# Kernel tuning notes

Hardware: AMD Instinct MI355X
Metric: run time of the kernel (lower is better)

## Reference

```python
import math
import jax, jax.numpy as jnp
import numpy as np

H = 4  # num heads
D = 512
MLP = 1024
EPS = 1e-6


def _ln(x, g, b):
    m = x.mean(-1, keepdims=True)
    v = ((x - m) ** 2).mean(-1, keepdims=True)
    return (x - m) / jnp.sqrt(v + EPS) * g + b


def _heads(x):
    B, S, d = x.shape
    return x.reshape(B, S, H, d // H).transpose(0, 2, 1, 3)  # [B,H,S,hd]


def _att(q, k, v, Wo, bo):
    # q,k,v: [B,S,D] already projected
    hd = q.shape[-1] // H
    qh, kh, vh = _heads(q), _heads(k), _heads(v)
    scores = jnp.einsum('bhqd,bhkd->bhqk', qh, kh) / math.sqrt(hd)
    probs = jax.nn.softmax(scores, axis=-1)
    ctx = jnp.einsum('bhqk,bhkd->bhqd', probs, vh)
    B, _, S, _ = ctx.shape
    ctx = ctx.transpose(0, 2, 1, 3).reshape(B, S, H * hd)
    return ctx @ Wo + bo


def setup_inputs() -> dict:
    key = jax.random.key(0)
    ks = jax.random.split(key, 32)
    i = iter(range(32))
    def w(shape, scale=0.02):
        return jax.random.normal(ks[next(i)], shape, dtype=jnp.float32) * scale
    inp = {
        'x1': jax.random.normal(ks[next(i)], (16, 1024, D), dtype=jnp.float32),
        'x2': jax.random.normal(ks[next(i)], (16, 1024, D), dtype=jnp.float32),
        'ln1_g': jnp.ones((D,), jnp.float32), 'ln1_b': jnp.zeros((D,), jnp.float32),
        'ln2_g': jnp.ones((D,), jnp.float32), 'ln2_b': jnp.zeros((D,), jnp.float32),
        'lnf_g': jnp.ones((D,), jnp.float32), 'lnf_b': jnp.zeros((D,), jnp.float32),
    }
    for name in ['q1', 'k1', 'v1', 'q2', 'k2', 'v2', 'q12', 'k12', 'v12', 'o']:
        inp['W' + name] = w((D, D))
        inp['b' + name] = jnp.zeros((D,), jnp.float32)
    inp['W1'] = w((D, MLP)); inp['b1'] = jnp.zeros((MLP,), jnp.float32)
    inp['W2'] = w((MLP, D)); inp['b2'] = jnp.zeros((D,), jnp.float32)
    return inp


def reference(x1, x2, ln1_g, ln1_b, ln2_g, ln2_b, lnf_g, lnf_b,
              Wq1, bq1, Wk1, bk1, Wv1, bv1,
              Wq2, bq2, Wk2, bk2, Wv2, bv2,
              Wq12, bq12, Wk12, bk12, Wv12, bv12,
              Wo, bo, W1, b1, W2, b2):
    identity = x1
    x1n = _ln(x1, ln1_g, ln1_b)
    x2n = _ln(x2, ln2_g, ln2_b)
    # stream-1 self-attention with residual onto normalized input
    src1 = x1n + _att(x1n @ Wq1 + bq1, x1n @ Wk1 + bk1, x1n @ Wv1 + bv1, Wo, bo)
    # stream-2 self-attention
    src2 = x2n + _att(x2n @ Wq2 + bq2, x2n @ Wk2 + bk2, x2n @ Wv2 + bv2, Wo, bo)
    # cross attention: query from src1, key/value from src2
    attn_out = _att(src1 @ Wq12 + bq12, src2 @ Wk12 + bk12, src2 @ Wv12 + bv12, Wo, bo)
    x = attn_out + identity
    h = _ln(x, lnf_g, lnf_b)
    h = jax.nn.gelu(h @ W1 + b1, approximate=False) @ W2 + b2
    return x + h
```

## Files before the change

### kernel.cpp

```cpp
#include <hip/hip_runtime.h>
#include <math.h>


#define SEQ   1024
#define DM    512
#define HDIM  128
#define MTOK  16384
#define MLPD  1024
#define SC2   ((float)(0.08838834764831845 * 1.4426950408889634))

typedef short bf16x8 __attribute__((ext_vector_type(8)));
typedef float f32x4  __attribute__((ext_vector_type(4)));
typedef float f32x16 __attribute__((ext_vector_type(16)));
typedef unsigned short us4 __attribute__((ext_vector_type(4)));

typedef unsigned int u32g __attribute__((address_space(1)));
typedef unsigned int u32l __attribute__((address_space(3)));

static __device__ __forceinline__ unsigned short f2b(float f) {
  union { float f; unsigned u; } v; v.f = f;
  unsigned r = v.u + 0x7FFFu + ((v.u >> 16) & 1u);
  return (unsigned short)(r >> 16);
}
static __device__ __forceinline__ float b2f(unsigned short h) {
  union { unsigned u; float f; } v; v.u = ((unsigned)h) << 16;
  return v.f;
}
static __device__ __forceinline__ unsigned pk2t(float a, float b) {
  union { float f; unsigned u; } va, vb; va.f = a; vb.f = b;
  return __builtin_amdgcn_perm(vb.u, va.u, 0x07060302u);
}
static __device__ __forceinline__ void gl_lds16(const void* g, void* l) {
  __builtin_amdgcn_global_load_lds((u32g*)g, (u32l*)l, 16, 0, 0);
}

struct P12 { const float* p[12]; };
struct P9  { const float* p[9]; };

__global__ __launch_bounds__(256) void prep_kernel(P12 ws, P9 bs,
                                                   unsigned short* __restrict__ WT0,
                                                   unsigned short* __restrict__ W1t,
                                                   unsigned short* __restrict__ W2t,
                                                   float* __restrict__ bcc) {
  int bid = blockIdx.x;
  if (bid >= 3584) {
    int i = (bid - 3584) * 256 + threadIdx.x;
    if (i < 4608) bcc[i] = bs.p[i >> 9][i & 511];
    return;
  }
  __shared__ float t[32][33];
  const float* W; unsigned short* Wt; int K, N, tt;
  if (bid < 2560)      { int wi = bid >> 8; W = ws.p[wi]; Wt = WT0 + (size_t)wi * 262144; K = 512; N = 512; tt = bid & 255; }
  else if (bid < 3072) { W = ws.p[10]; Wt = W1t; K = 512;  N = 1024; tt = bid - 2560; }
  else                 { W = ws.p[11]; Wt = W2t; K = 1024; N = 512;  tt = bid - 3072; }
  int ntiles = N >> 5;
  int bx = tt % ntiles, by = tt / ntiles;
  int n0 = bx * 32, k0 = by * 32;
  int tx = threadIdx.x & 31, ty = threadIdx.x >> 5;
#pragma unroll
  for (int i = 0; i < 32; i += 8)
    t[ty + i][tx] = W[(size_t)(k0 + ty + i) * N + n0 + tx];
  __syncthreads();
#pragma unroll
  for (int i = 0; i < 32; i += 8)
    Wt[(size_t)(n0 + ty + i) * K + k0 + tx] = f2b(t[tx][ty + i]);
}

__global__ __launch_bounds__(256) void ln_kernel(const float* __restrict__ X0,
                                                 const float* __restrict__ X1,
                                                 const float* __restrict__ g0w,
                                                 const float* __restrict__ b0w,
                                                 const float* __restrict__ g1w,
                                                 const float* __restrict__ b1w,
                                                 unsigned short* __restrict__ out0,
                                                 unsigned short* __restrict__ out1) {
  int idx  = blockIdx.x * 4 + (threadIdx.x >> 6);
  int sel  = idx >> 14;
  int row  = idx & 16383;
  const float* X = sel ? X1 : X0;
  const float* gw = sel ? g1w : g0w;
  const float* bw = sel ? b1w : b0w;
  unsigned short* outB = sel ? out1 : out0;
  int lane = threadIdx.x & 63;
  const float4* xr = (const float4*)(X + (size_t)row * DM);
  float4 a = xr[lane];
  float4 c = xr[lane + 64];
  float s  = a.x + a.y + a.z + a.w + c.x + c.y + c.z + c.w;
  float s2 = a.x*a.x + a.y*a.y + a.z*a.z + a.w*a.w
           + c.x*c.x + c.y*c.y + c.z*c.z + c.w*c.w;
#pragma unroll
  for (int off = 1; off < 64; off <<= 1) {
    s  += __shfl_xor(s,  off, 64);
    s2 += __shfl_xor(s2, off, 64);
  }
  float mean = s * (1.0f / 512.0f);
  float var  = s2 * (1.0f / 512.0f) - mean * mean;
  float rstd = rsqrtf(var + 1e-6f);
  const float4* gv = (const float4*)gw;
  const float4* bv = (const float4*)bw;
  float4 g1 = gv[lane], g2 = gv[lane + 64];
  float4 b1 = bv[lane], b2 = bv[lane + 64];
  us4 o1, o2;
  o1.x = f2b((a.x - mean) * rstd * g1.x + b1.x);
  o1.y = f2b((a.y - mean) * rstd * g1.y + b1.y);
  o1.z = f2b((a.z - mean) * rstd * g1.z + b1.z);
  o1.w = f2b((a.w - mean) * rstd * g1.w + b1.w);
  o2.x = f2b((c.x - mean) * rstd * g2.x + b2.x);
  o2.y = f2b((c.y - mean) * rstd * g2.y + b2.y);
  o2.z = f2b((c.z - mean) * rstd * g2.z + b2.z);
  o2.w = f2b((c.w - mean) * rstd * g2.w + b2.w);
  *(us4*)(outB + (size_t)row * DM + lane * 4)        = o1;
  *(us4*)(outB + (size_t)row * DM + (lane + 64) * 4) = o2;
}

template <int RES, bool GELU_ACT, int OMODE>
__global__ __launch_bounds__(256, 2) void gemm_kernel(const unsigned short* __restrict__ A,
                                                      const unsigned short* __restrict__ A1,
                                                      const unsigned short* __restrict__ Bt,
                                                      const float* __restrict__ bias,
                                                      const void* __restrict__ res,
                                                      float* __restrict__ outF,
                                                      unsigned short* __restrict__ outB,
                                                      unsigned short* __restrict__ outV,
                                                      int M, int N, int K) {
  int nT = N >> 7;
  int mT = M >> 7;
  int xcd = blockIdx.x & 7;
  int idx = blockIdx.x >> 3;
  int mPerX = mT >> 3;
  int q = idx / nT;
  int tm = xcd * mPerX + q;
  int tn = idx - q * nT;
  int m0 = tm << 7, n0 = tn << 7;
  int tid = threadIdx.x, lane = tid & 63, w = tid >> 6;
  int m16 = lane & 15, q4 = lane >> 4;
  int wr = (w & 1) << 6, wc = (w >> 1) << 6;
  __shared__ unsigned short Alds[2][128 * 64];
  __shared__ unsigned short Blds[2][128 * 64];
  f32x4 acc[4][4] = {};

  const unsigned short* Aeff = A;
  const unsigned short* Bteff = Bt;
  const float* biaseff = bias;
  if (OMODE == 3) {
    int half = tm >> 7;
    Bteff = Bt + (size_t)half * 3 * 262144;
    biaseff = bias + half * 1536;
  }
  if (OMODE == 4) {
    if (tn >= 4) Aeff = A1;
  }

  int srow = lane >> 3;
  int scol = ((lane & 7) ^ srow) << 3;
  const unsigned short* Ag = Aeff  + (size_t)(m0 + w * 8 + srow) * K + scol;
  const unsigned short* Bg = Bteff + (size_t)(n0 + w * 8 + srow) * K + scol;
  int ldst = w * 512;

#pragma unroll
  for (int it = 0; it < 4; ++it) {
    gl_lds16(Ag + (size_t)it * 32 * K, Alds[0] + it * 2048 + ldst);
    gl_lds16(Bg + (size_t)it * 32 * K, Blds[0] + it * 2048 + ldst);
  }

  int nk = K >> 6;
  for (int ks = 0; ks < nk; ++ks) {
    int cur = ks & 1, nxt = cur ^ 1;
    __syncthreads();
    if (ks + 1 < nk) {
      int k0n = (ks + 1) << 6;
#pragma unroll
      for (int it = 0; it < 4; ++it) {
        gl_lds16(Ag + (size_t)it * 32 * K + k0n, Alds[nxt] + it * 2048 + ldst);
        gl_lds16(Bg + (size_t)it * 32 * K + k0n, Blds[nxt] + it * 2048 + ldst);
      }
    }
    const unsigned short* Ar = Alds[cur];
    const unsigned short* Br = Blds[cur];
#pragma unroll
    for (int kk = 0; kk < 64; kk += 32) {
      bf16x8 af[4], bfr[4];
#pragma unroll
      for (int i = 0; i < 4; ++i) {
        int row = wr + i * 16 + m16;
        af[i] = *(const bf16x8*)(Ar + row * 64 + ((((kk >> 3) + q4) ^ (m16 & 7)) << 3));
      }
#pragma unroll
      for (int j = 0; j < 4; ++j) {
        int row = wc + j * 16 + m16;
        bfr[j] = *(const bf16x8*)(Br + row * 64 + ((((kk >> 3) + q4) ^ (m16 & 7)) << 3));
      }
#pragma unroll
      for (int i = 0; i < 4; ++i)
#pragma unroll
        for (int j = 0; j < 4; ++j)
          acc[i][j] = __builtin_amdgcn_mfma_f32_16x16x32_bf16(af[i], bfr[j], acc[i][j], 0, 0, 0);
    }
  }
  if (OMODE == 3 || OMODE == 4) {
    if (n0 < 1024) {
      int stride = (OMODE == 3) ? 1024 : 512;
      unsigned short* ob = outB;
      int coff = 0;
      if (OMODE == 4 && n0 >= 512) { ob = outB + (size_t)MTOK * 512; coff = 512; }
      float sc = (n0 < 512) ? SC2 : 1.0f;
#pragma unroll
      for (int i = 0; i < 4; ++i) {
#pragma unroll
        for (int r = 0; r < 4; ++r) {
          int row = m0 + wr + i * 16 + q4 * 4 + r;
#pragma unroll
          for (int j = 0; j < 4; ++j) {
            int col = n0 + wc + j * 16 + m16;
            ob[(size_t)row * stride + col - coff] = f2b((acc[i][j][r] + biaseff[col]) * sc);
          }
        }
      }
    } else {
#pragma unroll
      for (int i = 0; i < 4; ++i) {
        int row0 = m0 + wr + i * 16 + q4 * 4;
        int s = row0 & 1023, bl = row0 >> 10;
        s = (s & ~12) | ((s & 4) << 1) | ((s & 8) >> 1);
#pragma unroll
        for (int j = 0; j < 4; ++j) {
          int col = n0 + wc + j * 16 + m16;
          int hh = (col - 1024) >> 7, hd = col & 127;
          float bb = biaseff[col];
          us4 pkv;
          pkv.x = f2b(acc[i][j][0] + bb);
          pkv.y = f2b(acc[i][j][1] + bb);
          pkv.z = f2b(acc[i][j][2] + bb);
          pkv.w = f2b(acc[i][j][3] + bb);
          *(us4*)(outV + (((size_t)(bl * 4 + hh)) * HDIM + hd) * SEQ + s) = pkv;
        }
      }
    }
  } else {
#pragma unroll
    for (int i = 0; i < 4; ++i) {
#pragma unroll
      for (int r = 0; r < 4; ++r) {
        int row = m0 + wr + i * 16 + q4 * 4 + r;
#pragma unroll
        for (int j = 0; j < 4; ++j) {
          int col = n0 + wc + j * 16 + m16;
          float v = acc[i][j][r] + bias[col];
          if (RES == 1) v += ((const float*)res)[(size_t)row * N + col];
          if (RES == 2) v += b2f(((const unsigned short*)res)[(size_t)row * N + col]);
          if (GELU_ACT) v = 0.5f * v * (1.0f + erff(v * 0.70710678118654752f));
          if (OMODE == 1) outF[(size_t)row * N + col] = v;
          else            outB[(size_t)row * N + col] = f2b(v);
        }
      }
    }
  }
}

__global__ __launch_bounds__(256, 2) void attn_kernel(const unsigned short* __restrict__ Qb_,
                                                      const unsigned short* __restrict__ Kb_,
                                                      int tstride,
                                                      const unsigned short* __restrict__ Vt,
                                                      unsigned short* __restrict__ CTX,
                                                      int pairs_per_xcd) {
  int xcd = blockIdx.x & 7;
  int i   = blockIdx.x >> 3;
  int pair = xcd * pairs_per_xcd + (i >> 3);
  int qt   = i & 7;
  int b = pair >> 2, h = pair & 3;
  int tid = threadIdx.x, lane = tid & 63, w = tid >> 6;
  int m32 = lane & 31, hf = lane >> 5;
  size_t qkoff = ((size_t)b * SEQ) * tstride + h * HDIM;
  const unsigned short* Qg = Qb_ + qkoff;
  const unsigned short* Kg = Kb_ + qkoff;
  const unsigned short* Vp = Vt + (size_t)pair * HDIM * SEQ;

  __shared__ unsigned short Klds[2][64 * 128];
  __shared__ unsigned short Vlds[2][128 * 64];

  int qrow0 = qt * 128 + w * 32;
  bf16x8 qf[8];
  {
    const unsigned short* qp = Qg + (size_t)(qrow0 + m32) * tstride + hf * 8;
#pragma unroll
    for (int ks = 0; ks < 8; ++ks) qf[ks] = *(const bf16x8*)(qp + ks * 16);
  }
  bf16x8 onesf;
#pragma unroll
  for (int j = 0; j < 8; ++j) onesf[j] = (short)0x3F80;

  const unsigned short* kp0 = Kg + (size_t)(16 * w + (lane >> 4)) * tstride
                              + (((lane & 15) ^ (lane >> 4)) << 3);
  const unsigned short* kp1 = Kg + (size_t)(16 * w + 4 + (lane >> 4)) * tstride
                              + (((lane & 15) ^ ((lane >> 4) + 4)) << 3);
  const unsigned short* vp0 = Vp + (size_t)(32 * w + (lane >> 3)) * SEQ
                              + (((lane & 7) ^ (lane >> 3)) << 3);
  int klo = 16 * w * 128;
  int vlo = 32 * w * 64;

  gl_lds16(kp0,               Klds[0] + klo);
  gl_lds16(kp1,               Klds[0] + klo + 4 * 128);
  gl_lds16(kp0 + 8 * tstride, Klds[0] + klo + 8 * 128);
  gl_lds16(kp1 + 8 * tstride, Klds[0] + klo + 12 * 128);
  gl_lds16(vp0,               Vlds[0] + vlo);
  gl_lds16(vp0 + 8 * SEQ,     Vlds[0] + vlo + 8 * 64);
  gl_lds16(vp0 + 16 * SEQ,    Vlds[0] + vlo + 16 * 64);
  gl_lds16(vp0 + 24 * SEQ,    Vlds[0] + vlo + 24 * 64);

  f32x16 o0 = {}, o1 = {}, o2 = {}, o3 = {};
  f32x16 lacc = {};

  for (int kt = 0; kt < 16; ++kt) {
    int cur = kt & 1, nxt = cur ^ 1;
    __syncthreads();
    if (kt < 15) {
      kp0 += 64 * tstride; kp1 += 64 * tstride; vp0 += 64;
      gl_lds16(kp0,               Klds[nxt] + klo);
      gl_lds16(kp1,               Klds[nxt] + klo + 4 * 128);
      gl_lds16(kp0 + 8 * tstride, Klds[nxt] + klo + 8 * 128);
      gl_lds16(kp1 + 8 * tstride, Klds[nxt] + klo + 12 * 128);
      gl_lds16(vp0,               Vlds[nxt] + vlo);
      gl_lds16(vp0 + 8 * SEQ,     Vlds[nxt] + vlo + 8 * 64);
      gl_lds16(vp0 + 16 * SEQ,    Vlds[nxt] + vlo + 16 * 64);
      gl_lds16(vp0 + 24 * SEQ,    Vlds[nxt] + vlo + 24 * 64);
    }
    const unsigned short* Kr = Klds[cur];
    const unsigned short* Vr = Vlds[cur];

    f32x16 sc0 = {}, sc1 = {};
#pragma unroll
    for (int ks = 0; ks < 8; ++ks) {
      int ch = 2 * ks + hf;
      bf16x8 kf0 = *(const bf16x8*)(Kr + m32 * 128 + ((ch ^ (m32 & 7)) << 3));
      sc0 = __builtin_amdgcn_mfma_f32_32x32x16_bf16(kf0, qf[ks], sc0, 0, 0, 0);
      int k1r = 32 + m32;
      bf16x8 kf1 = *(const bf16x8*)(Kr + k1r * 128 + ((ch ^ (k1r & 7)) << 3));
      sc1 = __builtin_amdgcn_mfma_f32_32x32x16_bf16(kf1, qf[ks], sc1, 0, 0, 0);
    }

    bf16x8 pa[4];
#pragma unroll
    for (int t = 0; t < 2; ++t) {
      const f32x16& sc = t ? sc1 : sc0;
#pragma unroll
      for (int g = 0; g < 2; ++g) {
        union { unsigned u[4]; bf16x8 v; } uu;
        uu.u[0] = pk2t(exp2f(sc[8*g+0]), exp2f(sc[8*g+1]));
        uu.u[1] = pk2t(exp2f(sc[8*g+2]), exp2f(sc[8*g+3]));
        uu.u[2] = pk2t(exp2f(sc[8*g+4]), exp2f(sc[8*g+5]));
        uu.u[3] = pk2t(exp2f(sc[8*g+6]), exp2f(sc[8*g+7]));
        pa[2*t + g] = uu.v;
      }
    }

#pragma unroll
    for (int ks = 0; ks < 4; ++ks) {
      int ch = 2 * ks + hf;
      int sw = m32 & 7;
      lacc = __builtin_amdgcn_mfma_f32_32x32x16_bf16(pa[ks], onesf, lacc, 0, 0, 0);
      {
        bf16x8 vf = *(const bf16x8*)(Vr + m32 * 64 + ((ch ^ sw) << 3));
        o0 = __builtin_amdgcn_mfma_f32_32x32x16_bf16(pa[ks], vf, o0, 0, 0, 0);
      }
      {
        bf16x8 vf = *(const bf16x8*)(Vr + (32 + m32) * 64 + ((ch ^ sw) << 3));
        o1 = __builtin_amdgcn_mfma_f32_32x32x16_bf16(pa[ks], vf, o1, 0, 0, 0);
      }
      {
        bf16x8 vf = *(const bf16x8*)(Vr + (64 + m32) * 64 + ((ch ^ sw) << 3));
        o2 = __builtin_amdgcn_mfma_f32_32x32x16_bf16(pa[ks], vf, o2, 0, 0, 0);
      }
      {
        bf16x8 vf = *(const bf16x8*)(Vr + (96 + m32) * 64 + ((ch ^ sw) << 3));
        o3 = __builtin_amdgcn_mfma_f32_32x32x16_bf16(pa[ks], vf, o3, 0, 0, 0);
      }
    }
  }

  size_t obase = ((size_t)b * SEQ + qrow0) * DM + h * HDIM;
#pragma unroll
  for (int g = 0; g < 4; ++g) {
#pragma unroll
    for (int r = 0; r < 4; ++r) {
      int reg = 4 * g + r;
      int rowl = 8 * g + 4 * hf + r;
      float inv = 1.0f / lacc[reg];
      size_t off = obase + (size_t)rowl * DM + m32;
      CTX[off]      = f2b(o0[reg] * inv);
      CTX[off + 32] = f2b(o1[reg] * inv);
      CTX[off + 64] = f2b(o2[reg] * inv);
      CTX[off + 96] = f2b(o3[reg] * inv);
    }
  }
}

extern "C" void kernel_launch(void* const* d_in, const int* in_sizes, int n_in,
                              void* d_out, int out_size, void* d_ws, size_t ws_size,
                              hipStream_t stream) {
  const float* x1    = (const float*)d_in[0];
  const float* x2    = (const float*)d_in[1];
  const float* ln1_g = (const float*)d_in[2];
  const float* ln1_b = (const float*)d_in[3];
  const float* ln2_g = (const float*)d_in[4];
  const float* ln2_b = (const float*)d_in[5];
  const float* lnf_g = (const float*)d_in[6];
  const float* lnf_b = (const float*)d_in[7];
  P12 wsrc;
  for (int i = 0; i < 10; ++i) wsrc.p[i] = (const float*)d_in[8 + 2 * i];
  wsrc.p[10] = (const float*)d_in[28];
  wsrc.p[11] = (const float*)d_in[30];
  P9 bsrc;
  for (int i = 0; i < 9; ++i) bsrc.p[i] = (const float*)d_in[9 + 2 * i];
  const float* bo   = (const float*)d_in[27];
  const float* b1   = (const float*)d_in[29];
  const float* b2   = (const float*)d_in[31];

  char* ws = (char*)d_ws;
  size_t off = 0;
  auto alloc = [&](size_t bytes) -> char* {
    char* p = ws + off;
    off += (bytes + 255) & ~(size_t)255;
    return p;
  };
  unsigned short* WT0 = (unsigned short*)alloc((size_t)10 * 512 * 512 * 2);
  auto WT = [&](int i) { return WT0 + (size_t)i * 262144; };
  unsigned short* W1t = (unsigned short*)alloc((size_t)1024 * 512 * 2);
  unsigned short* W2t = (unsigned short*)alloc((size_t)512 * 1024 * 2);
  float*          bcc = (float*)alloc(4608 * 4);
  unsigned short* XN  = (unsigned short*)alloc((size_t)2 * MTOK * DM * 2);
  unsigned short* QKb = (unsigned short*)alloc((size_t)2 * MTOK * 1024 * 2);
  unsigned short* Vtb = (unsigned short*)alloc((size_t)128 * HDIM * SEQ * 2);
  unsigned short* CT  = (unsigned short*)alloc((size_t)2 * MTOK * DM * 2);
  float*          Xf  = (float*)alloc((size_t)MTOK * DM * 4);
  unsigned short* XN1 = XN + (size_t)MTOK * DM;
  unsigned short* MID = QKb;
  unsigned short* HN  = Vtb;
  float* bias_self  = bcc;
  float* bias_cross = bcc + 3072;

  prep_kernel<<<3602, 256, 0, stream>>>(wsrc, bsrc, WT0, W1t, W2t, bcc);

  ln_kernel<<<2 * MTOK / 4, 256, 0, stream>>>(x1, x2, ln1_g, ln1_b, ln2_g, ln2_b, XN, XN1);

  gemm_kernel<0, false, 3><<<3072, 256, 0, stream>>>(XN, nullptr, WT0, bias_self,
      nullptr, nullptr, QKb, Vtb, 32768, 1536, 512);

  attn_kernel<<<128 * 8, 256, 0, stream>>>(QKb, QKb + 512, 1024, Vtb, CT, 16);

  gemm_kernel<2, false, 0><<<1024, 256, 0, stream>>>(CT, nullptr, WT(9), bo, XN,
      nullptr, XN, nullptr, 32768, 512, 512);

  gemm_kernel<0, false, 4><<<1536, 256, 0, stream>>>(XN, XN1, WT(6), bias_cross,
      nullptr, nullptr, QKb, Vtb, 16384, 1536, 512);

  attn_kernel<<<64 * 8, 256, 0, stream>>>(QKb, QKb + (size_t)MTOK * 512, 512, Vtb, CT, 8);

  gemm_kernel<1, false, 1><<<512, 256, 0, stream>>>(CT, nullptr, WT(9), bo, x1,
      Xf, nullptr, nullptr, 16384, 512, 512);

  ln_kernel<<<MTOK / 4, 256, 0, stream>>>(Xf, Xf, lnf_g, lnf_b, lnf_g, lnf_b, HN, HN);

  gemm_kernel<0, true,  0><<<1024, 256, 0, stream>>>(HN, nullptr, W1t, b1,
      nullptr, nullptr, MID, nullptr, 16384, 1024, 512);
  gemm_kernel<1, false, 1><<<512, 256, 0, stream>>>(MID, nullptr, W2t, b2,
      Xf, (float*)d_out, nullptr, nullptr, 16384, 512, 1024);
}
```

Before: 520.0 us.

## Halve attention KV tile to raise occupancy and add MFMA priority hints

The attention kernel's key/value tile per iteration drops from 64 to 32 keys, which halves the double-buffered LDS footprint and shrinks score registers. Launch bounds rise from 2 to 4 blocks per SIMD, and the LDS load mapping and V swizzle are reworked for the narrower tile. s_setprio hints are placed around the MFMA sections so waves doing matrix math get scheduling priority. The cost is twice as many loop iterations and __syncthreads barriers, and the tighter register budget may cause spills.

```diff
diff --git a/kernel.cpp b/kernel.cpp
--- a/kernel.cpp
+++ b/kernel.cpp
@@ -257,7 +257,7 @@
   }
 }
 
-__global__ __launch_bounds__(256, 2) void attn_kernel(const unsigned short* __restrict__ Qb_,
+__global__ __launch_bounds__(256, 4) void attn_kernel(const unsigned short* __restrict__ Qb_,
                                                       const unsigned short* __restrict__ Kb_,
                                                       int tstride,
                                                       const unsigned short* __restrict__ Vt,
@@ -275,8 +275,8 @@
   const unsigned short* Kg = Kb_ + qkoff;
   const unsigned short* Vp = Vt + (size_t)pair * HDIM * SEQ;
 
-  __shared__ unsigned short Klds[2][64 * 128];
-  __shared__ unsigned short Vlds[2][128 * 64];
+  __shared__ unsigned short Klds[2][32 * 128];
+  __shared__ unsigned short Vlds[2][128 * 32];
 
   int qrow0 = qt * 128 + w * 32;
   bf16x8 qf[8];
@@ -289,92 +289,81 @@
 #pragma unroll
   for (int j = 0; j < 8; ++j) onesf[j] = (short)0x3F80;
 
-  const unsigned short* kp0 = Kg + (size_t)(16 * w + (lane >> 4)) * tstride
+  const unsigned short* kpA = Kg + (size_t)(8 * w + (lane >> 4)) * tstride
                               + (((lane & 15) ^ (lane >> 4)) << 3);
-  const unsigned short* kp1 = Kg + (size_t)(16 * w + 4 + (lane >> 4)) * tstride
-                              + (((lane & 15) ^ ((lane >> 4) + 4)) << 3);
-  const unsigned short* vp0 = Vp + (size_t)(32 * w + (lane >> 3)) * SEQ
-                              + (((lane & 7) ^ (lane >> 3)) << 3);
-  int klo = 16 * w * 128;
-  int vlo = 32 * w * 64;
-
-  gl_lds16(kp0,               Klds[0] + klo);
-  gl_lds16(kp1,               Klds[0] + klo + 4 * 128);
-  gl_lds16(kp0 + 8 * tstride, Klds[0] + klo + 8 * 128);
-  gl_lds16(kp1 + 8 * tstride, Klds[0] + klo + 12 * 128);
-  gl_lds16(vp0,               Vlds[0] + vlo);
-  gl_lds16(vp0 + 8 * SEQ,     Vlds[0] + vlo + 8 * 64);
-  gl_lds16(vp0 + 16 * SEQ,    Vlds[0] + vlo + 16 * 64);
-  gl_lds16(vp0 + 24 * SEQ,    Vlds[0] + vlo + 24 * 64);
+  const unsigned short* kpB = Kg + (size_t)(8 * w + 4 + (lane >> 4)) * tstride
+                              + (((lane & 15) ^ (4 + (lane >> 4))) << 3);
+  const unsigned short* vpA = Vp + (size_t)(32 * w + (lane >> 2)) * SEQ
+                              + (((lane & 3) ^ ((lane >> 3) & 3)) << 3);
+  int klo = w * 1024;
+  int vlo = w * 1024;
+
+  gl_lds16(kpA,            Klds[0] + klo);
+  gl_lds16(kpB,            Klds[0] + klo + 512);
+  gl_lds16(vpA,            Vlds[0] + vlo);
+  gl_lds16(vpA + 16 * SEQ, Vlds[0] + vlo + 512);
 
   f32x16 o0 = {}, o1 = {}, o2 = {}, o3 = {};
   f32x16 lacc = {};
 
-  for (int kt = 0; kt < 16; ++kt) {
+  for (int kt = 0; kt < 32; ++kt) {
     int cur = kt & 1, nxt = cur ^ 1;
     __syncthreads();
-    if (kt < 15) {
-      kp0 += 64 * tstride; kp1 += 64 * tstride; vp0 += 64;
-      gl_lds16(kp0,               Klds[nxt] + klo);
-      gl_lds16(kp1,               Klds[nxt] + klo + 4 * 128);
-      gl_lds16(kp0 + 8 * tstride, Klds[nxt] + klo + 8 * 128);
-      gl_lds16(kp1 + 8 * tstride, Klds[nxt] + klo + 12 * 128);
-      gl_lds16(vp0,               Vlds[nxt] + vlo);
-      gl_lds16(vp0 + 8 * SEQ,     Vlds[nxt] + vlo + 8 * 64);
-      gl_lds16(vp0 + 16 * SEQ,    Vlds[nxt] + vlo + 16 * 64);
-      gl_lds16(vp0 + 24 * SEQ,    Vlds[nxt] + vlo + 24 * 64);
+    if (kt < 31) {
+      kpA += 32 * tstride; kpB += 32 * tstride; vpA += 32;
+      gl_lds16(kpA,            Klds[nxt] + klo);
+      gl_lds16(kpB,            Klds[nxt] + klo + 512);
+      gl_lds16(vpA,            Vlds[nxt] + vlo);
+      gl_lds16(vpA + 16 * SEQ, Vlds[nxt] + vlo + 512);
     }
     const unsigned short* Kr = Klds[cur];
     const unsigned short* Vr = Vlds[cur];
 
-    f32x16 sc0 = {}, sc1 = {};
+    __builtin_amdgcn_s_setprio(1);
+    f32x16 sc0 = {};
 #pragma unroll
     for (int ks = 0; ks < 8; ++ks) {
       int ch = 2 * ks + hf;
       bf16x8 kf0 = *(const bf16x8*)(Kr + m32 * 128 + ((ch ^ (m32 & 7)) << 3));
       sc0 = __builtin_amdgcn_mfma_f32_32x32x16_bf16(kf0, qf[ks], sc0, 0, 0, 0);
-      int k1r = 32 + m32;
-      bf16x8 kf1 = *(const bf16x8*)(Kr + k1r * 128 + ((ch ^ (k1r & 7)) << 3));
-      sc1 = __builtin_amdgcn_mfma_f32_32x32x16_bf16(kf1, qf[ks], sc1, 0, 0, 0);
-    }
-
-    bf16x8 pa[4];
-#pragma unroll
-    for (int t = 0; t < 2; ++t) {
-      const f32x16& sc = t ? sc1 : sc0;
-#pragma unroll
-      for (int g = 0; g < 2; ++g) {
-        union { unsigned u[4]; bf16x8 v; } uu;
-        uu.u[0] = pk2t(exp2f(sc[8*g+0]), exp2f(sc[8*g+1]));
-        uu.u[1] = pk2t(exp2f(sc[8*g+2]), exp2f(sc[8*g+3]));
-        uu.u[2] = pk2t(exp2f(sc[8*g+4]), exp2f(sc[8*g+5]));
-        uu.u[3] = pk2t(exp2f(sc[8*g+6]), exp2f(sc[8*g+7]));
-        pa[2*t + g] = uu.v;
-      }
-    }
-
-#pragma unroll
-    for (int ks = 0; ks < 4; ++ks) {
+    }
+    __builtin_amdgcn_s_setprio(0);
+
+    bf16x8 pa[2];
+#pragma unroll
+    for (int g = 0; g < 2; ++g) {
+      union { unsigned u[4]; bf16x8 v; } uu;
+      uu.u[0] = pk2t(exp2f(sc0[8*g+0]), exp2f(sc0[8*g+1]));
+      uu.u[1] = pk2t(exp2f(sc0[8*g+2]), exp2f(sc0[8*g+3]));
+      uu.u[2] = pk2t(exp2f(sc0[8*g+4]), exp2f(sc0[8*g+5]));
+      uu.u[3] = pk2t(exp2f(sc0[8*g+6]), exp2f(sc0[8*g+7]));
+      pa[g] = uu.v;
+    }
+
+    __builtin_amdgcn_s_setprio(1);
+#pragma unroll
+    for (int ks = 0; ks < 2; ++ks) {
       int ch = 2 * ks + hf;
-      int sw = m32 & 7;
+      int vsw = (m32 >> 1) & 3;
       lacc = __builtin_amdgcn_mfma_f32_32x32x16_bf16(pa[ks], onesf, lacc, 0, 0, 0);
       {
-        bf16x8 vf = *(const bf16x8*)(Vr + m32 * 64 + ((ch ^ sw) << 3));
+        bf16x8 vf = *(const bf16x8*)(Vr + m32 * 32 + ((ch ^ vsw) << 3));
         o0 = __builtin_amdgcn_mfma_f32_32x32x16_bf16(pa[ks], vf, o0, 0, 0, 0);
       }
       {
-        bf16x8 vf = *(const bf16x8*)(Vr + (32 + m32) * 64 + ((ch ^ sw) << 3));
+        bf16x8 vf = *(const bf16x8*)(Vr + (32 + m32) * 32 + ((ch ^ vsw) << 3));
         o1 = __builtin_amdgcn_mfma_f32_32x32x16_bf16(pa[ks], vf, o1, 0, 0, 0);
       }
       {
-        bf16x8 vf = *(const bf16x8*)(Vr + (64 + m32) * 64 + ((ch ^ sw) << 3));
+        bf16x8 vf = *(const bf16x8*)(Vr + (64 + m32) * 32 + ((ch ^ vsw) << 3));
         o2 = __builtin_amdgcn_mfma_f32_32x32x16_bf16(pa[ks], vf, o2, 0, 0, 0);
       }
       {
-        bf16x8 vf = *(const bf16x8*)(Vr + (96 + m32) * 64 + ((ch ^ sw) << 3));
+        bf16x8 vf = *(const bf16x8*)(Vr + (96 + m32) * 32 + ((ch ^ vsw) << 3));
         o3 = __builtin_amdgcn_mfma_f32_32x32x16_bf16(pa[ks], vf, o3, 0, 0, 0);
       }
     }
+    __builtin_amdgcn_s_setprio(0);
   }
 
   size_t obase = ((size_t)b * SEQ + qrow0) * DM + h * HDIM;
```

New measurement: 710.8 us. 36.7% more time.
